# Kernel optimization log

Measured on AMD Instinct MI355X. Metric: run time of the kernel, lower is better.

Reference implementation:

```python
import jax, jax.numpy as jnp
import numpy as np

N, T, V, D = 32, 417, 25, 2
NODES = T * V            # 10425 nodes per sample graph
E = 80000                # static interframe edges, shared across batch
HID = 20                 # GCN hidden size
LH = 50                  # lstm hidden == d_model == fc_hidden
NH, FF, NL = 5, 2048, 3  # transformer heads / ffn dim / layers
CO = 85                  # conv1d out channels (in_channels == T)
NC = 6
NS = 2                   # n stacked (lstm, gcn) stages
SZ = int(T * 0.2)        # 83 sampled timesteps for loss1
EPS = 1e-5


def setup_inputs() -> dict:
    key = jax.random.key(0)
    ks = iter(jax.random.split(key, 80))
    def r(shape, s=0.1):
        return jax.random.normal(next(ks), shape, dtype=jnp.float32) * s
    inp = {
        "x": jax.random.normal(next(ks), (N, T, V * D), dtype=jnp.float32),
        "y": jax.random.randint(next(ks), (N,), 0, NC),
        "edge_index": jax.random.randint(next(ks), (2, E), 0, NODES),
        "idx2": jax.random.randint(next(ks), (N, SZ), 0, T - 1),
        "h0s": jax.random.normal(next(ks), (NS, N, LH), dtype=jnp.float32),
        "c0s": jax.random.normal(next(ks), (NS, N, LH), dtype=jnp.float32),
        # params; layouts are (in, out) so x @ W == torch x @ W.T
        "lstm_Wih": r((NS, LH, 4 * LH)),
        "lstm_Whh": r((NS, LH, 4 * LH)),
        "lstm_bih": r((NS, 4 * LH)),
        "lstm_bhh": r((NS, 4 * LH)),
        "gcn1_W": r((NS, D, HID)),
        "gcn1_b": r((NS, HID)),
        "bn_g": jnp.ones((NS, HID), jnp.float32),
        "bn_b": jnp.zeros((NS, HID), jnp.float32),
        "gcn2_W": r((NS, HID, D)),
        "gcn2_b": r((NS, D)),
        "fc_W": r((LH, LH)),
        "fc_b": r((LH,)),
        "conv_W": r((CO, T)),
        "conv_b": r((CO,)),
        "attn_inW": r((NL, LH, 3 * LH)),
        "attn_inb": r((NL, 3 * LH)),
        "attn_outW": r((NL, LH, LH)),
        "attn_outb": r((NL, LH)),
        "ff1W": r((NL, LH, FF)),
        "ff1b": r((NL, FF)),
        "ff2W": r((NL, FF, LH)),
        "ff2b": r((NL, LH)),
        "ln1g": jnp.ones((NL, LH), jnp.float32),
        "ln1b": jnp.zeros((NL, LH), jnp.float32),
        "ln2g": jnp.ones((NL, LH), jnp.float32),
        "ln2b": jnp.zeros((NL, LH), jnp.float32),
        "Wc1": r((CO * LH, LH), 0.02),
        "bc1": r((LH,)),
        "Wc2": r((LH, NC)),
        "bc2": r((NC,)),
    }
    return inp


def _lstm(x, Wih, Whh, bih, bhh, h0, c0):
    # x: (N,T,in); single layer, batch_first; gate order i,f,g,o (torch)
    def step(carry, xt):
        h, c = carry
        g = xt @ Wih + h @ Whh + bih + bhh
        i, f, gg, o = jnp.split(g, 4, axis=-1)
        c = jax.nn.sigmoid(f) * c + jax.nn.sigmoid(i) * jnp.tanh(gg)
        h = jax.nn.sigmoid(o) * jnp.tanh(c)
        return (h, c), h
    _, hs = jax.lax.scan(step, (h0, c0), jnp.swapaxes(x, 0, 1))
    return jnp.swapaxes(hs, 0, 1)


def _gcn(X, W, b, src, dst, norm):
    # PyG GCNConv: x @ W, symmetric-normalized mean over neighbors (+self loops), + bias
    H = X @ W                                   # (N, NODES, out)
    msg = H[:, src, :] * norm[None, :, None]    # (N, E+NODES, out)
    agg = jax.vmap(lambda m: jax.ops.segment_sum(m, dst, num_segments=NODES))(msg)
    return agg + b


def _ln(x, g, b):
    m = x.mean(-1, keepdims=True)
    v = ((x - m) ** 2).mean(-1, keepdims=True)
    return (x - m) * jax.lax.rsqrt(v + EPS) * g + b


def _mha(x, inW, inb, outW, outb):
    # torch batch_first=False semantics: x is (S, B, E); here S=N, B=CO
    S, B, Em = x.shape
    hd = Em // NH
    qkv = x @ inW + inb
    q, k, v = jnp.split(qkv, 3, axis=-1)
    q = q.reshape(S, B, NH, hd)
    k = k.reshape(S, B, NH, hd)
    v = v.reshape(S, B, NH, hd)
    att = jnp.einsum('sbhd,tbhd->bhst', q, k) * (jnp.float32(hd) ** -0.5)
    w = jax.nn.softmax(att, axis=-1)
    o = jnp.einsum('bhst,tbhd->sbhd', w, v).reshape(S, B, Em)
    return o @ outW + outb


def _forward(x, y, edge_index, idx2, h0s, c0s,
             lstm_Wih, lstm_Whh, lstm_bih, lstm_bhh,
             gcn1_W, gcn1_b, bn_g, bn_b, gcn2_W, gcn2_b,
             fc_W, fc_b, conv_W, conv_b,
             attn_inW, attn_inb, attn_outW, attn_outb,
             ff1W, ff1b, ff2W, ff2b, ln1g, ln1b, ln2g, ln2b,
             Wc1, bc1, Wc2, bc2):
    loops = jnp.arange(NODES)
    src = jnp.concatenate([edge_index[0], loops])
    dst = jnp.concatenate([edge_index[1], loops])
    deg = jax.ops.segment_sum(jnp.ones(src.shape[0], jnp.float32), dst, num_segments=NODES)
    dinv = jnp.where(deg > 0, deg ** -0.5, 0.0)
    norm = dinv[src] * dinv[dst]

    x1 = x
    for s in range(NS):
        x1 = _lstm(x1, lstm_Wih[s], lstm_Whh[s], lstm_bih[s], lstm_bhh[s], h0s[s], c0s[s])
        xg = x1.reshape(N, NODES, D)
        h = _gcn(xg, gcn1_W[s], gcn1_b[s], src, dst, norm)
        # BatchNorm1d over all nodes of the whole batched graph (training stats)
        hf = h.reshape(-1, HID)
        m = hf.mean(0)
        v = hf.var(0)
        h = (h - m) * jax.lax.rsqrt(v + EPS) * bn_g[s] + bn_b[s]
        h = jax.nn.relu(h)
        xg = _gcn(h, gcn2_W[s], gcn2_b[s], src, dst, norm)
        x1 = xg.reshape(N, T, V * D)

    # unsupervised next-frame loss (Dropout is eval-mode identity)
    x_b1 = x1 @ fc_W + fc_b
    rows = jnp.arange(N)[:, None]
    pred = x_b1[rows, idx2]
    tgt = x[rows, idx2 + 1]
    loss1 = jnp.mean((pred - tgt) ** 2)

    # Conv1d(417->85, k=1) over time-as-channels
    t = jnp.einsum('oc,ncl->nol', conv_W, x1) + conv_b[None, :, None]  # (N, CO, LH)
    # torch encoder treats dim0=N as sequence, dim1=CO as batch (post-norm layers)
    for l in range(NL):
        a = _mha(t, attn_inW[l], attn_inb[l], attn_outW[l], attn_outb[l])
        t = _ln(t + a, ln1g[l], ln1b[l])
        f = jax.nn.relu(t @ ff1W[l] + ff1b[l]) @ ff2W[l] + ff2b[l]
        t = _ln(t + f, ln2g[l], ln2b[l])

    flat = t.reshape(N, CO * LH)
    h1 = jax.nn.relu(flat @ Wc1 + bc1)
    logits = h1 @ Wc2 + bc2
    logp = jax.nn.log_softmax(logits, axis=-1)
    loss2 = -jnp.mean(logp[jnp.arange(N), y])
    return jnp.exp(logp), loss1, loss2


def reference(x, y, edge_index, idx2, h0s, c0s,
              lstm_Wih, lstm_Whh, lstm_bih, lstm_bhh,
              gcn1_W, gcn1_b, bn_g, bn_b, gcn2_W, gcn2_b,
              fc_W, fc_b, conv_W, conv_b,
              attn_inW, attn_inb, attn_outW, attn_outb,
              ff1W, ff1b, ff2W, ff2b, ln1g, ln1b, ln2g, ln2b,
              Wc1, bc1, Wc2, bc2):
    return _forward(x, y, edge_index, idx2, h0s, c0s,
                    lstm_Wih, lstm_Whh, lstm_bih, lstm_bhh,
                    gcn1_W, gcn1_b, bn_g, bn_b, gcn2_W, gcn2_b,
                    fc_W, fc_b, conv_W, conv_b,
                    attn_inW, attn_inb, attn_outW, attn_outb,
                    ff1W, ff1b, ff2W, ff2b, ln1g, ln1b, ln2g, ln2b,
                    Wc1, bc1, Wc2, bc2)
```

## Files before the change

kernel.cpp:

```cpp
#include <hip/hip_runtime.h>
#include <math.h>

#define N_ 32
#define T_ 417
#define V_ 25
#define D_ 2
#define NODES_ 10425
#define E_ 80000
#define EN_ (E_ + NODES_)
#define HID_ 20
#define LH_ 50
#define NH_ 5
#define HD_ 10
#define FF_ 2048
#define NL_ 3
#define CO_ 85
#define NC_ 6
#define NS_ 2
#define SZ_ 83
#define EPS_ 1e-5f
#define NCH_ 11
#define NBNB_ 1304

__device__ inline float sane(float v){
  return (v == v && fabsf(v) < 1e30f) ? v : 0.f;
}

__device__ inline float wave_sum(float v){
  #pragma unroll
  for (int off = 32; off > 0; off >>= 1) v += __shfl_xor(v, off, 64);
  return v;
}

__global__ void k_init(const float* __restrict__ x, float* __restrict__ x1,
                       int* __restrict__ deg, float* __restrict__ accs){
  int i = blockIdx.x * 256 + threadIdx.x;
  if (i < N_*T_*LH_) x1[i] = x[i];
  if (i < NODES_) deg[i] = 0;
  if (i < 8) accs[i] = 0.f;
}

__global__ void k_deg(const int* __restrict__ ei, int* __restrict__ deg){
  int e = blockIdx.x * 256 + threadIdx.x;
  if (e >= EN_) return;
  int d = (e < E_) ? ei[E_ + e] : (e - E_);
  if ((unsigned)d >= NODES_) d = 0;
  atomicAdd(&deg[d], 1);
}

__global__ __launch_bounds__(256) void k_chunksum(const int* __restrict__ deg, int* __restrict__ csum){
  __shared__ int red[256];
  int chunk = blockIdx.x, tid = threadIdx.x;
  int s = 0;
  for (int i = tid; i < 1024; i += 256){
    int g = chunk*1024 + i;
    s += (g < NODES_) ? deg[g] : 0;
  }
  red[tid] = s;
  __syncthreads();
  for (int off = 128; off > 0; off >>= 1){
    if (tid < off) red[tid] += red[tid + off];
    __syncthreads();
  }
  if (tid == 0) csum[chunk] = red[0];
}

__global__ void k_chunkscan(int* __restrict__ csum){
  if (threadIdx.x == 0 && blockIdx.x == 0){
    int run = 0;
    for (int i = 0; i < NCH_; i++){ int t = csum[i]; csum[i] = run; run += t; }
  }
}

__global__ __launch_bounds__(1024) void k_scan2(const int* __restrict__ deg, const int* __restrict__ csum,
                       int* __restrict__ rowoff, int* __restrict__ wp, float* __restrict__ dinv){
  __shared__ int sdata[1024];
  int chunk = blockIdx.x, tid = threadIdx.x;
  int g = chunk*1024 + tid;
  int v = (g < NODES_) ? deg[g] : 0;
  int xv = v;
  sdata[tid] = xv;
  __syncthreads();
  for (int off = 1; off < 1024; off <<= 1){
    int add = (tid >= off) ? sdata[tid - off] : 0;
    __syncthreads();
    xv += add;
    sdata[tid] = xv;
    __syncthreads();
  }
  if (g < NODES_){
    int excl = csum[chunk] + xv - v;
    rowoff[g] = excl;
    wp[g] = excl;
    dinv[g] = (v > 0) ? rsqrtf((float)v) : 0.f;
  }
}

__global__ void k_scatter(const int* __restrict__ ei, const float* __restrict__ dinv,
                          int* __restrict__ wp, int* __restrict__ col, float* __restrict__ val){
  int e = blockIdx.x * 256 + threadIdx.x;
  if (e >= EN_) return;
  int s, d;
  if (e < E_){ s = ei[e]; d = ei[E_ + e]; } else { s = d = e - E_; }
  if ((unsigned)s >= NODES_) s = 0;
  if ((unsigned)d >= NODES_) d = 0;
  int pos = atomicAdd(&wp[d], 1);
  if ((unsigned)pos < EN_){
    col[pos] = s;
    val[pos] = dinv[s] * dinv[d];
  }
}

__global__ void k_xw(const float* __restrict__ x1, const float* __restrict__ Wih,
                     const float* __restrict__ bih, const float* __restrict__ bhh,
                     float* __restrict__ xW, int s){
  int idx = blockIdx.x * 256 + threadIdx.x;
  if (idx >= N_*T_*200) return;
  int r = idx / 200, g = idx % 200;
  const float* W = Wih + s*LH_*200;
  const float* xr = x1 + r*LH_;
  float acc = bih[s*200+g] + bhh[s*200+g];
  #pragma unroll 10
  for (int k = 0; k < LH_; k++) acc += xr[k] * W[k*200 + g];
  xW[idx] = acc;
}

__global__ __launch_bounds__(256) void k_lstm(const float* __restrict__ xW, float* __restrict__ x1,
                       const float* __restrict__ Whh, const float* __restrict__ h0,
                       const float* __restrict__ c0, int s){
  __shared__ float hs[LH_];
  __shared__ float gates[200];
  int n = blockIdx.x, tid = threadIdx.x;
  int gcol = (tid < 200) ? tid : 0;
  float wcol[LH_];
  {
    const float* W = Whh + s*LH_*200 + gcol;
    #pragma unroll
    for (int k = 0; k < LH_; k++) wcol[k] = W[k*200];
  }
  float c = 0.f;
  if (tid < LH_){
    c = c0[s*N_*LH_ + n*LH_ + tid];
    hs[tid] = h0[s*N_*LH_ + n*LH_ + tid];
  }
  __syncthreads();
  const float* xwn = xW + (size_t)n*T_*200;
  float* out = x1 + (size_t)n*T_*LH_;
  for (int t = 0; t < T_; t++){
    if (tid < 200){
      float acc = xwn[t*200 + tid];
      #pragma unroll
      for (int k = 0; k < LH_; k++) acc += hs[k] * wcol[k];
      gates[tid] = acc;
    }
    __syncthreads();
    if (tid < LH_){
      float gi = gates[tid], gf = gates[LH_+tid], gg = gates[100+tid], go = gates[150+tid];
      float si = 1.f/(1.f + __expf(-gi));
      float sf = 1.f/(1.f + __expf(-gf));
      float so = 1.f/(1.f + __expf(-go));
      float tg = tanhf(gg);
      c = sf*c + si*tg;
      float h = so * tanhf(c);
      hs[tid] = h;
      out[t*LH_ + tid] = h;
    }
    __syncthreads();
  }
}

__global__ void k_tonode(const float* __restrict__ x1, float* __restrict__ P0){
  int idx = blockIdx.x * 256 + threadIdx.x;
  if (idx >= NODES_*64) return;
  int v = idx >> 6, rem = idx & 63;
  int n = rem >> 1, d = rem & 1;
  P0[idx] = x1[n*(T_*LH_) + v*D_ + d];
}

__global__ __launch_bounds__(64) void k_gather(const int* __restrict__ rowoff, const int* __restrict__ deg,
                       const int* __restrict__ col, const float* __restrict__ val,
                       const float* __restrict__ src, float* __restrict__ dst){
  int v = blockIdx.x, tid = threadIdx.x;
  int start = rowoff[v], len = deg[v];
  float acc = 0.f;
  for (int j = 0; j < len; j++){
    int cs = col[start + j];
    if ((unsigned)cs >= NODES_) cs = 0;
    acc += val[start + j] * src[cs*64 + tid];
  }
  dst[v*64 + tid] = acc;
}

__global__ __launch_bounds__(256) void k_bnstat(const float* __restrict__ P1, float* __restrict__ bnpart){
  int idx = blockIdx.x * 256 + threadIdx.x;
  float p0 = 0.f, p1v = 0.f;
  if (idx < NODES_*N_){ p0 = P1[idx*2]; p1v = P1[idx*2+1]; }
  float sv[5] = {p0, p1v, p0*p0, p1v*p1v, p0*p1v};
  __shared__ float red[5][4];
  int wave = threadIdx.x >> 6, lane = threadIdx.x & 63;
  #pragma unroll
  for (int j = 0; j < 5; j++){
    float w = wave_sum(sv[j]);
    if (lane == 0) red[j][wave] = w;
  }
  __syncthreads();
  if (threadIdx.x < 5){
    int j = threadIdx.x;
    bnpart[j*NBNB_ + blockIdx.x] = red[j][0] + red[j][1] + red[j][2] + red[j][3];
  }
}

__global__ __launch_bounds__(256) void k_bnfin(const float* __restrict__ bnpart,
                        const float* __restrict__ W1, const float* __restrict__ b1,
                        const float* __restrict__ bn_g, const float* __restrict__ bn_b,
                        float* __restrict__ bnsc, int s){
  __shared__ float red[256];
  __shared__ float S[5];
  int tid = threadIdx.x;
  for (int j = 0; j < 5; j++){
    float acc = 0.f;
    for (int t = tid; t < NBNB_; t += 256) acc += bnpart[j*NBNB_ + t];
    red[tid] = acc;
    __syncthreads();
    for (int off = 128; off > 0; off >>= 1){
      if (tid < off) red[tid] += red[tid + off];
      __syncthreads();
    }
    if (tid == 0) S[j] = red[0];
    __syncthreads();
  }
  if (tid < HID_){
    int c = tid;
    const float M = (float)(N_*NODES_);
    float w0 = W1[s*D_*HID_ + c], w1 = W1[s*D_*HID_ + HID_ + c];
    float bc = b1[s*HID_ + c];
    float m0 = S[0]/M, m1 = S[1]/M;
    float e00 = S[2]/M, e11 = S[3]/M, e01 = S[4]/M;
    float mean = w0*m0 + w1*m1 + bc;
    float v00 = e00 - m0*m0, v11 = e11 - m1*m1, c01 = e01 - m0*m1;
    float var = w0*w0*v00 + w1*w1*v11 + 2.f*w0*w1*c01;
    var = fmaxf(var, 0.f);
    float sc = bn_g[s*HID_ + c] * rsqrtf(var + EPS_);
    bnsc[c] = sc;
    bnsc[HID_ + c] = bn_b[s*HID_ + c] - mean*sc;
  }
}

__global__ __launch_bounds__(256) void k_bnrelu_t2(const float* __restrict__ P1, const float* __restrict__ bnsc,
                            const float* __restrict__ W1, const float* __restrict__ b1,
                            const float* __restrict__ W2, float* __restrict__ Rb, int s){
  int idx = blockIdx.x * 256 + threadIdx.x;
  if (idx >= NODES_*N_) return;
  float p0 = P1[idx*2], p1v = P1[idx*2+1];
  const float* W1p = W1 + s*D_*HID_;
  const float* W2p = W2 + s*HID_*D_;
  float a0 = 0.f, a1 = 0.f;
  #pragma unroll
  for (int c = 0; c < HID_; c++){
    float q = p0*W1p[c] + p1v*W1p[HID_ + c] + b1[s*HID_ + c];
    float h = fmaxf(q*bnsc[c] + bnsc[HID_ + c], 0.f);
    a0 += h * W2p[c*D_];
    a1 += h * W2p[c*D_ + 1];
  }
  Rb[idx*2]     = a0;
  Rb[idx*2 + 1] = a1;
}

__global__ __launch_bounds__(64) void k_gcn2(const int* __restrict__ rowoff, const int* __restrict__ deg,
                      const int* __restrict__ col, const float* __restrict__ val,
                      const float* __restrict__ Rb, const float* __restrict__ gb2,
                      float* __restrict__ x1, int s){
  int v = blockIdx.x, tid = threadIdx.x;
  int start = rowoff[v], len = deg[v];
  float acc = 0.f;
  for (int j = 0; j < len; j++){
    int cs = col[start + j];
    if ((unsigned)cs >= NODES_) cs = 0;
    acc += val[start + j] * Rb[cs*64 + tid];
  }
  int n = tid >> 1, d = tid & 1;
  x1[n*(T_*LH_) + v*D_ + d] = acc + gb2[s*D_ + d];
}

__global__ __launch_bounds__(64) void k_loss1(const float* __restrict__ x1, const float* __restrict__ x,
                       const int* __restrict__ idx2, const float* __restrict__ fcW,
                       const float* __restrict__ fcb, float* __restrict__ accs){
  int bi = blockIdx.x;
  int n = bi / SZ_, j = bi % SZ_;
  int row = idx2[n*SZ_ + j];
  if ((unsigned)row >= (T_ - 1)) row = 0;
  int l = threadIdx.x;
  float sq = 0.f;
  if (l < LH_){
    const float* xr = x1 + n*T_*LH_ + row*LH_;
    float acc = fcb[l];
    #pragma unroll 10
    for (int k = 0; k < LH_; k++) acc += xr[k] * fcW[k*LH_ + l];
    float dd = acc - x[n*T_*LH_ + (row+1)*LH_ + l];
    sq = dd*dd;
  }
  sq = wave_sum(sq);
  if (l == 0) atomicAdd(&accs[0], sq);
}

__global__ __launch_bounds__(64) void k_conv(const float* __restrict__ x1, const float* __restrict__ cW,
                      const float* __restrict__ cb, float* __restrict__ tb){
  int bi = blockIdx.x;
  int n = bi / CO_, o = bi % CO_;
  int l = threadIdx.x;
  if (l >= LH_) return;
  float acc = cb[o];
  const float* w = cW + o*T_;
  const float* xr = x1 + n*T_*LH_ + l;
  #pragma unroll 4
  for (int c2 = 0; c2 < T_; c2++) acc += w[c2] * xr[c2*LH_];
  tb[bi*LH_ + l] = acc;
}

__global__ void k_qkv(const float* __restrict__ tb, const float* __restrict__ inW,
                      const float* __restrict__ inb, float* __restrict__ qkv, int l3){
  int idx = blockIdx.x * 256 + threadIdx.x;
  if (idx >= N_*CO_*150) return;
  int r = idx / 150, j = idx % 150;
  const float* W = inW + l3*LH_*150;
  const float* tr = tb + r*LH_;
  float acc = inb[l3*150 + j];
  #pragma unroll 10
  for (int k = 0; k < LH_; k++) acc += tr[k] * W[k*150 + j];
  qkv[idx] = acc;
}

__global__ __launch_bounds__(128) void k_attn(const float* __restrict__ qkv, float* __restrict__ abuf){
  __shared__ float qs[32][HD_], ks[32][HD_], vs[32][HD_], att[32][32];
  int bi = blockIdx.x;
  int b = bi % CO_, h = bi / CO_;
  int tid = threadIdx.x;
  for (int idx = tid; idx < 960; idx += 128){
    int grp = idx / 320, m = idx % 320, ss = m / HD_, dd = m % HD_;
    float vvv = qkv[(ss*CO_ + b)*150 + grp*LH_ + h*HD_ + dd];
    if (grp == 0) qs[ss][dd] = vvv;
    else if (grp == 1) ks[ss][dd] = vvv;
    else vs[ss][dd] = vvv;
  }
  __syncthreads();
  const float scale = 0.31622776601683794f;
  for (int idx = tid; idx < 1024; idx += 128){
    int ss = idx >> 5, tt = idx & 31;
    float a = 0.f;
    #pragma unroll
    for (int dd = 0; dd < HD_; dd++) a += qs[ss][dd]*ks[tt][dd];
    att[ss][tt] = a*scale;
  }
  __syncthreads();
  if (tid < 32){
    float m = -1e31f;
    for (int tt = 0; tt < 32; tt++) m = fmaxf(m, att[tid][tt]);
    float sum = 0.f;
    for (int tt = 0; tt < 32; tt++){ float e = __expf(att[tid][tt] - m); att[tid][tt] = e; sum += e; }
    float inv = 1.f / fmaxf(sum, 1e-30f);
    for (int tt = 0; tt < 32; tt++) att[tid][tt] *= inv;
  }
  __syncthreads();
  for (int idx = tid; idx < 320; idx += 128){
    int ss = idx / HD_, dd = idx % HD_;
    float acc = 0.f;
    #pragma unroll
    for (int tt = 0; tt < 32; tt++) acc += att[ss][tt]*vs[tt][dd];
    abuf[(ss*CO_ + b)*LH_ + h*HD_ + dd] = acc;
  }
}

__global__ __launch_bounds__(64) void k_proj_ln(float* __restrict__ tb, const float* __restrict__ abuf,
                         const float* __restrict__ outW, const float* __restrict__ outb,
                         const float* __restrict__ g, const float* __restrict__ bb, int l3){
  __shared__ float orow[LH_];
  int r = blockIdx.x, l = threadIdx.x;
  if (l < LH_) orow[l] = abuf[r*LH_ + l];
  __syncthreads();
  float rr = 0.f;
  if (l < LH_){
    const float* W = outW + l3*LH_*LH_;
    float p = outb[l3*LH_ + l];
    #pragma unroll 10
    for (int k = 0; k < LH_; k++) p += orow[k] * W[k*LH_ + l];
    rr = tb[r*LH_ + l] + p;
  }
  float mean = wave_sum(rr) / (float)LH_;
  float dv = (l < LH_) ? (rr - mean) : 0.f;
  float var = wave_sum(dv*dv) / (float)LH_;
  if (l < LH_)
    tb[r*LH_ + l] = (rr - mean)*rsqrtf(var + EPS_)*g[l3*LH_ + l] + bb[l3*LH_ + l];
}

__global__ __launch_bounds__(512) void k_ff(float* __restrict__ tb, const float* __restrict__ w1,
                     const float* __restrict__ bi1, const float* __restrict__ w2,
                     const float* __restrict__ bi2, const float* __restrict__ g,
                     const float* __restrict__ bb, int l3){
  __shared__ float tin[2][LH_];
  __shared__ float hb0[FF_], hb1[FF_];
  __shared__ float part[2][8][LH_];
  int r0 = blockIdx.x * 2, tid = threadIdx.x;
  if (tid < 2*LH_) tin[tid/LH_][tid%LH_] = tb[r0*LH_ + tid];
  __syncthreads();
  const float* W1l = w1 + l3*LH_*FF_;
  #pragma unroll
  for (int i = 0; i < 4; i++){
    int j = i*512 + tid;
    float bj = bi1[l3*FF_ + j];
    float a0 = bj, a1 = bj;
    #pragma unroll 10
    for (int k = 0; k < LH_; k++){
      float w = W1l[k*FF_ + j];
      a0 += tin[0][k]*w;
      a1 += tin[1][k]*w;
    }
    hb0[j] = fmaxf(a0, 0.f);
    hb1[j] = fmaxf(a1, 0.f);
  }
  __syncthreads();
  const float* W2l = w2 + l3*FF_*LH_;
  int l = tid & 63, grp = tid >> 6;
  if (l < LH_){
    float a0 = 0.f, a1 = 0.f;
    int jbase = grp * 256;
    const float* wp = W2l + (size_t)jbase*LH_ + l;
    #pragma unroll 4
    for (int jj = 0; jj < 256; jj++){
      float w = wp[jj*LH_];
      a0 += hb0[jbase + jj]*w;
      a1 += hb1[jbase + jj]*w;
    }
    part[0][grp][l] = a0;
    part[1][grp][l] = a1;
  }
  __syncthreads();
  if (tid < 128){
    int row = tid >> 6, ll = tid & 63;
    float out = 0.f;
    if (ll < LH_){
      float a = 0.f;
      #pragma unroll
      for (int gg = 0; gg < 8; gg++) a += part[row][gg][ll];
      out = a + bi2[l3*LH_ + ll] + tin[row][ll];
    }
    float s1 = (ll < LH_) ? out : 0.f;
    float mean = wave_sum(s1) / (float)LH_;
    float dv = (ll < LH_) ? (out - mean) : 0.f;
    float var = wave_sum(dv*dv) / (float)LH_;
    if (ll < LH_)
      tb[(r0 + row)*LH_ + ll] = (out - mean)*rsqrtf(var + EPS_)*g[l3*LH_ + ll] + bb[l3*LH_ + ll];
  }
}

__global__ __launch_bounds__(512) void k_head(const float* __restrict__ tb, const int* __restrict__ y,
                       const float* __restrict__ Wc1, const float* __restrict__ bc1,
                       const float* __restrict__ Wc2, const float* __restrict__ bc2,
                       float* __restrict__ out, float* __restrict__ accs){
  __shared__ float part[8][LH_];
  __shared__ float h1[LH_];
  __shared__ float lgs[NC_];
  int n = blockIdx.x, tid = threadIdx.x;
  int l = tid & 63, grp = tid >> 6;
  const float* tr = tb + n*CO_*LH_;
  if (l < LH_){
    int k0 = grp * 532;
    int k1 = k0 + 532; if (k1 > CO_*LH_) k1 = CO_*LH_;
    float acc = 0.f;
    for (int k = k0; k < k1; k++) acc += tr[k] * Wc1[k*LH_ + l];
    part[grp][l] = acc;
  }
  __syncthreads();
  if (tid < LH_){
    float a = bc1[tid];
    #pragma unroll
    for (int gg = 0; gg < 8; gg++) a += part[gg][tid];
    h1[tid] = fmaxf(a, 0.f);
  }
  __syncthreads();
  if (tid < NC_){
    float a = bc2[tid];
    #pragma unroll 10
    for (int k = 0; k < LH_; k++) a += h1[k] * Wc2[k*NC_ + tid];
    lgs[tid] = a;
  }
  __syncthreads();
  if (tid == 0){
    float m = -1e31f;
    for (int c2 = 0; c2 < NC_; c2++) m = fmaxf(m, lgs[c2]);
    float sum = 0.f;
    for (int c2 = 0; c2 < NC_; c2++) sum += __expf(lgs[c2] - m);
    float lse = m + logf(fmaxf(sum, 1e-30f));
    for (int c2 = 0; c2 < NC_; c2++)
      out[n*NC_ + c2] = __expf(lgs[c2] - lse);
    int yy = y[n];
    if ((unsigned)yy >= NC_) yy = 0;
    atomicAdd(&accs[1], -(lgs[yy] - lse));
  }
}

__global__ void k_fin(const float* __restrict__ accs, float* __restrict__ out){
  if (threadIdx.x == 0 && blockIdx.x == 0){
    out[N_*NC_]     = sane(accs[0] / (float)(N_*SZ_*LH_));
    out[N_*NC_ + 1] = sane(accs[1] / (float)N_);
  }
}

extern "C" void kernel_launch(void* const* d_in, const int* in_sizes, int n_in,
                              void* d_out, int out_size, void* d_ws, size_t ws_size,
                              hipStream_t stream){
  static const int expect[36] = {
    667200, 32, 160000, 2656, 3200, 3200,
    20000, 20000, 400, 400,
    80, 40, 40, 40, 80, 4,
    2500, 50, 35445, 85,
    22500, 450, 7500, 150,
    307200, 6144, 307200, 150,
    150, 150, 150, 150,
    212500, 50, 300, 6
  };
  if (n_in != 36 || out_size != 194 || ws_size < 14300000) return;
  for (int i = 0; i < 36; i++) if (in_sizes[i] != expect[i]) return;

  const float* x        = (const float*)d_in[0];
  const int*   y        = (const int*)d_in[1];
  const int*   ei       = (const int*)d_in[2];
  const int*   idx2     = (const int*)d_in[3];
  const float* h0s      = (const float*)d_in[4];
  const float* c0s      = (const float*)d_in[5];
  const float* lstm_Wih = (const float*)d_in[6];
  const float* lstm_Whh = (const float*)d_in[7];
  const float* lstm_bih = (const float*)d_in[8];
  const float* lstm_bhh = (const float*)d_in[9];
  const float* gcn1_W   = (const float*)d_in[10];
  const float* gcn1_b   = (const float*)d_in[11];
  const float* bn_g     = (const float*)d_in[12];
  const float* bn_b     = (const float*)d_in[13];
  const float* gcn2_W   = (const float*)d_in[14];
  const float* gcn2_b   = (const float*)d_in[15];
  const float* fc_W     = (const float*)d_in[16];
  const float* fc_b     = (const float*)d_in[17];
  const float* conv_W   = (const float*)d_in[18];
  const float* conv_b   = (const float*)d_in[19];
  const float* attn_inW = (const float*)d_in[20];
  const float* attn_inb = (const float*)d_in[21];
  const float* attn_outW= (const float*)d_in[22];
  const float* attn_outb= (const float*)d_in[23];
  const float* ff1W     = (const float*)d_in[24];
  const float* ff1b     = (const float*)d_in[25];
  const float* ff2W     = (const float*)d_in[26];
  const float* ff2b     = (const float*)d_in[27];
  const float* ln1g     = (const float*)d_in[28];
  const float* ln1b     = (const float*)d_in[29];
  const float* ln2g     = (const float*)d_in[30];
  const float* ln2b     = (const float*)d_in[31];
  const float* Wc1      = (const float*)d_in[32];
  const float* bc1      = (const float*)d_in[33];
  const float* Wc2      = (const float*)d_in[34];
  const float* bc2      = (const float*)d_in[35];
  float* out = (float*)d_out;

  char* wsp = (char*)d_ws;
  size_t off = 0;
  auto alloc = [&](size_t bytes)->void*{
    void* p = wsp + off;
    off = (off + bytes + 255) & ~(size_t)255;
    return p;
  };
  float* x1   = (float*)alloc((size_t)N_*T_*LH_*4);
  float* X    = (float*)alloc((size_t)N_*T_*200*4);
  float* val  = (float*)alloc((size_t)EN_*4);
  float* dinv = (float*)alloc((size_t)NODES_*4);
  float* bnsc = (float*)alloc(64*4);
  float* accs = (float*)alloc(8*4);
  int*   deg  = (int*)alloc((size_t)NODES_*4);
  int*   rowoff = (int*)alloc((size_t)(NODES_+1)*4);
  int*   wp   = (int*)alloc((size_t)NODES_*4);
  int*   col  = (int*)alloc((size_t)EN_*4);
  int*   csum = (int*)alloc(16*4);
  float* xW     = X;
  float* P0     = X;
  float* P1     = X + (size_t)NODES_*64;
  float* bnpart = X + (size_t)2*NODES_*64;
  float* Rb     = P0;
  float* tb     = X;
  float* qkvb   = X + 136064;
  float* abuf   = X + 544128;

  k_init<<<dim3((N_*T_*LH_ + 255)/256), dim3(256), 0, stream>>>(x, x1, deg, accs);
  k_deg<<<dim3((EN_ + 255)/256), dim3(256), 0, stream>>>(ei, deg);
  k_chunksum<<<dim3(NCH_), dim3(256), 0, stream>>>(deg, csum);
  k_chunkscan<<<dim3(1), dim3(64), 0, stream>>>(csum);
  k_scan2<<<dim3(NCH_), dim3(1024), 0, stream>>>(deg, csum, rowoff, wp, dinv);
  k_scatter<<<dim3((EN_ + 255)/256), dim3(256), 0, stream>>>(ei, dinv, wp, col, val);

  for (int s = 0; s < NS_; s++){
    k_xw<<<dim3((N_*T_*200 + 255)/256), dim3(256), 0, stream>>>(x1, lstm_Wih, lstm_bih, lstm_bhh, xW, s);
    k_lstm<<<dim3(N_), dim3(256), 0, stream>>>(xW, x1, lstm_Whh, h0s, c0s, s);
    k_tonode<<<dim3((NODES_*64 + 255)/256), dim3(256), 0, stream>>>(x1, P0);
    k_gather<<<dim3(NODES_), dim3(64), 0, stream>>>(rowoff, deg, col, val, P0, P1);
    k_bnstat<<<dim3(NBNB_), dim3(256), 0, stream>>>(P1, bnpart);
    k_bnfin<<<dim3(1), dim3(256), 0, stream>>>(bnpart, gcn1_W, gcn1_b, bn_g, bn_b, bnsc, s);
    k_bnrelu_t2<<<dim3((N_*NODES_ + 255)/256), dim3(256), 0, stream>>>(P1, bnsc, gcn1_W, gcn1_b, gcn2_W, Rb, s);
    k_gcn2<<<dim3(NODES_), dim3(64), 0, stream>>>(rowoff, deg, col, val, Rb, gcn2_b, x1, s);
  }

  k_loss1<<<dim3(N_*SZ_), dim3(64), 0, stream>>>(x1, x, idx2, fc_W, fc_b, accs);
  k_conv<<<dim3(N_*CO_), dim3(64), 0, stream>>>(x1, conv_W, conv_b, tb);

  for (int l3 = 0; l3 < NL_; l3++){
    k_qkv<<<dim3((N_*CO_*150 + 255)/256), dim3(256), 0, stream>>>(tb, attn_inW, attn_inb, qkvb, l3);
    k_attn<<<dim3(NH_*CO_), dim3(128), 0, stream>>>(qkvb, abuf);
    k_proj_ln<<<dim3(N_*CO_), dim3(64), 0, stream>>>(tb, abuf, attn_outW, attn_outb, ln1g, ln1b, l3);
    k_ff<<<dim3(N_*CO_/2), dim3(512), 0, stream>>>(tb, ff1W, ff1b, ff2W, ff2b, ln2g, ln2b, l3);
  }

  k_head<<<dim3(N_), dim3(512), 0, stream>>>(tb, y, Wc1, bc1, Wc2, bc2, out, accs);
  k_fin<<<dim3(1), dim3(64), 0, stream>>>(accs, out);
}
```

Measured before the change: 1.514 ms.

## Restructure LSTM recurrence with per-wave redundant cell state and shuffles

The LSTM kernel now assigns one gate block to each of four 64-lane waves. Every wave computes the cell update redundantly, so the hidden state stays in registers and is broadcast with wave shuffles instead of going through shared memory. A double-buffered gate array removes one of the two block barriers per timestep, and the next timestep's input projection is prefetched into a register. This shortens the serial dependency chain of the 417-step recurrence, at the cost of duplicated transcendental work in each wave.

```diff
diff --git a/kernel.cpp b/kernel.cpp
--- a/kernel.cpp
+++ b/kernel.cpp
@@ -128,44 +128,46 @@
 __global__ __launch_bounds__(256) void k_lstm(const float* __restrict__ xW, float* __restrict__ x1,
                        const float* __restrict__ Whh, const float* __restrict__ h0,
                        const float* __restrict__ c0, int s){
-  __shared__ float hs[LH_];
-  __shared__ float gates[200];
+  __shared__ float gbuf[2][200];
   int n = blockIdx.x, tid = threadIdx.x;
-  int gcol = (tid < 200) ? tid : 0;
+  int w = tid >> 6;
+  int l = tid & 63;
+  int li = (l < LH_) ? l : 0;
   float wcol[LH_];
   {
-    const float* W = Whh + s*LH_*200 + gcol;
+    const float* W = Whh + s*LH_*200 + w*LH_ + li;
     #pragma unroll
     for (int k = 0; k < LH_; k++) wcol[k] = W[k*200];
   }
-  float c = 0.f;
-  if (tid < LH_){
-    c = c0[s*N_*LH_ + n*LH_ + tid];
-    hs[tid] = h0[s*N_*LH_ + n*LH_ + tid];
-  }
-  __syncthreads();
+  float h = 0.f, c = 0.f;
+  if (l < LH_){
+    h = h0[s*N_*LH_ + n*LH_ + l];
+    c = c0[s*N_*LH_ + n*LH_ + l];
+  }
   const float* xwn = xW + (size_t)n*T_*200;
   float* out = x1 + (size_t)n*T_*LH_;
+  float xnext = (l < LH_) ? xwn[w*LH_ + li] : 0.f;
   for (int t = 0; t < T_; t++){
-    if (tid < 200){
-      float acc = xwn[t*200 + tid];
-      #pragma unroll
-      for (int k = 0; k < LH_; k++) acc += hs[k] * wcol[k];
-      gates[tid] = acc;
+    float acc = xnext;
+    if (t + 1 < T_) xnext = (l < LH_) ? xwn[(t+1)*200 + w*LH_ + li] : 0.f;
+    #pragma unroll
+    for (int k = 0; k < LH_; k++){
+      float hk = __shfl(h, k, 64);
+      acc += hk * wcol[k];
     }
+    if (l < LH_) gbuf[t & 1][w*LH_ + l] = acc;
     __syncthreads();
-    if (tid < LH_){
-      float gi = gates[tid], gf = gates[LH_+tid], gg = gates[100+tid], go = gates[150+tid];
+    if (l < LH_){
+      const float* gb = gbuf[t & 1];
+      float gi = gb[l], gf = gb[LH_+l], gg = gb[100+l], go = gb[150+l];
       float si = 1.f/(1.f + __expf(-gi));
       float sf = 1.f/(1.f + __expf(-gf));
       float so = 1.f/(1.f + __expf(-go));
       float tg = tanhf(gg);
       c = sf*c + si*tg;
-      float h = so * tanhf(c);
-      hs[tid] = h;
-      out[t*LH_ + tid] = h;
+      h = so * tanhf(c);
+      if (w == 0) out[t*LH_ + l] = h;
     }
-    __syncthreads();
   }
 }
 
```

New measurement: 1.676 ms. +10.7%, slower.
